# Performance work log

Hardware: AMD Instinct MI355X
Metric: run time of the kernel (lower is better)

Reference implementation:

```python
import jax, jax.numpy as jnp
import numpy as np
from jax import lax

N, H, W = 8, 64, 64
SX1, SX2, THX, TLX = 256, 256, 256, 256
E1, E2, A1, OT = 256, 64, 128, 256
EBD = SX2 // 2            # ebd_factor=2
TXC = THX + TLX           # 512
IN1 = SX1 + TXC           # 768
BV = EBD + TXC            # 640


def upsample2x_align_corners(x):
    # bilinear, align_corners=True, scale_factor=2 (matches nn.Upsample)
    n, c, h, w = x.shape
    ho, wo = 2 * h, 2 * w
    ys = jnp.linspace(0.0, h - 1.0, ho)
    xs = jnp.linspace(0.0, w - 1.0, wo)
    y0 = jnp.floor(ys).astype(jnp.int32); y1 = jnp.minimum(y0 + 1, h - 1)
    x0 = jnp.floor(xs).astype(jnp.int32); x1 = jnp.minimum(x0 + 1, w - 1)
    wy = (ys - y0).astype(x.dtype); wx = (xs - x0).astype(x.dtype)
    xh = x[:, :, y0, :] * (1.0 - wy)[None, None, :, None] + x[:, :, y1, :] * wy[None, None, :, None]
    return xh[:, :, :, x0] * (1.0 - wx) + xh[:, :, :, x1] * wx


def conv1x1(x, w, b=None):
    # x: [N,C,H,W], w: [O,C]
    y = jnp.einsum('nchw,oc->nohw', x, w)
    if b is not None:
        y = y + b[None, :, None, None]
    return y


def conv3x3(x, w, b):
    y = lax.conv_general_dilated(x, w, window_strides=(1, 1), padding=((1, 1), (1, 1)),
                                 dimension_numbers=('NCHW', 'OIHW', 'NCHW'))
    return y + b[None, :, None, None]


def setup_inputs() -> dict:
    key = jax.random.key(0)
    ks = jax.random.split(key, 20)
    g = lambda k, shape, fan: jax.random.normal(k, shape, jnp.float32) * np.sqrt(2.0 / fan)
    return {
        'sx1': jax.random.normal(ks[0], (N, SX1, H, W), jnp.float32),
        'sx2': jax.random.normal(ks[1], (N, SX2, H, W), jnp.float32),
        't_hx': jax.random.normal(ks[2], (N, THX, H, W), jnp.float32),
        'tx': jax.random.normal(ks[3], (N, TLX, H // 2, W // 2), jnp.float32),
        'W_t1': g(ks[4], (E1, IN1), IN1 + E1), 'b_t1': jnp.zeros((E1,), jnp.float32),
        'W_t2': g(ks[5], (E2, E1), E1 + E2),
        'W_t3': g(ks[6], (SX2, E2), E2 + SX2),
        'W_U': g(ks[7], (SX2, SX2), 2 * SX2), 'b_U': jnp.zeros((SX2,), jnp.float32),
        'W_V': g(ks[8], (EBD, SX2), SX2 + EBD), 'b_V': jnp.zeros((EBD,), jnp.float32),
        'W_a1': g(ks[9], (A1, BV), BV + A1), 'b_a1': jnp.zeros((A1,), jnp.float32),
        'W_a2': g(ks[10], (BV, A1), A1 + BV), 'b_a2': jnp.zeros((BV,), jnp.float32),
        'W_ot': g(ks[11], (OT, BV, 3, 3), 9 * (BV + OT)), 'b_ot': jnp.zeros((OT,), jnp.float32),
    }


def reference(sx1, sx2, t_hx, tx, W_t1, b_t1, W_t2, W_t3, W_U, b_U, W_V, b_V,
              W_a1, b_a1, W_a2, b_a2, W_ot, b_ot):
    tx_up = upsample2x_align_corners(tx)
    txc = jnp.concatenate([t_hx, tx_up], axis=1)          # [N,TXC,H,W]
    st = jnp.concatenate([sx1, txc], axis=1)              # [N,IN1,H,W]
    w = jax.nn.relu(conv1x1(st, W_t1, b_t1))
    w = jnp.mean(w, axis=(2, 3), keepdims=True)           # GAP -> [N,E1,1,1]
    w = jax.nn.relu(conv1x1(w, W_t2))
    w = conv1x1(w, W_t3)                                  # [N,SX2,1,1]
    norm = jnp.sqrt(jnp.sum(w * w, axis=1, keepdims=True))
    w = w / jnp.maximum(norm, 1e-12)                      # F.normalize(dim=1)
    b = jax.nn.relu(conv1x1(sx2, W_U, b_U))
    b = b * w                                             # AdaptiveConv2d grouped 1x1 == per-sample per-channel scale
    b = jax.nn.relu(conv1x1(b, W_V, b_V))
    b = jnp.concatenate([b, txc], axis=1)                 # [N,BV,H,W]
    a = jax.nn.relu(conv1x1(b, W_a1, b_a1))
    a = jax.nn.sigmoid(conv1x1(a, W_a2, b_a2))
    a = a * b
    a = jax.nn.relu(conv3x3(a, W_ot, b_ot))               # [N,OT,H,W]
    return (a, w)
```

## Files before the change

kernel.cpp:

```cpp
#include <hip/hip_runtime.h>
#include <hip/hip_bf16.h>

#define PP 4096
#define HH 64
#define WW 64

typedef __attribute__((ext_vector_type(8))) short short8b;
typedef __attribute__((ext_vector_type(4))) float f32x4;

static __device__ __forceinline__ float bf2f(short s) {
    union { unsigned int u; float f; } cv; cv.u = ((unsigned int)(unsigned short)s) << 16; return cv.f;
}
static __device__ __forceinline__ short f2bf(float f) {
    __hip_bfloat16 h = __float2bfloat16(f);
    return *reinterpret_cast<short*>(&h);
}

static __device__ __forceinline__ void pack16(const float* __restrict__ W,
                                              short* __restrict__ dst,
                                              int MT, int K, int s) {
    int total = MT * 2 * (K / 64) * 64;
    if (s >= total) return;
    int lane = s & 63;
    int rest = s >> 6;
    int ks = rest & 1; rest >>= 1;
    int mt = rest % MT;
    int cc = rest / MT;
    int o   = mt * 16 + (lane & 15);
    int ch0 = cc * 64 + ks * 32 + (lane >> 4) * 8;
    short8b v;
    #pragma unroll
    for (int j = 0; j < 8; ++j) v[j] = f2bf(W[(size_t)o * K + ch0 + j]);
    ((short8b*)dst)[s] = v;
}

__global__ void k_packall(const float* __restrict__ Wt1, const float* __restrict__ WU,
                          const float* __restrict__ WV, const float* __restrict__ Wa1,
                          const float* __restrict__ Wa2, const float* __restrict__ Wot,
                          short* __restrict__ Wt1p, short* __restrict__ WUp,
                          short* __restrict__ WVp, short* __restrict__ Wa1p,
                          short* __restrict__ Wa2p, short* __restrict__ Wotp) {
    int b = blockIdx.x, tid = threadIdx.x;
    if (b < 96)       { pack16(Wt1, Wt1p, 16, 768, (b)       * 256 + tid); }
    else if (b < 128) { pack16(WU,  WUp,  16, 256, (b - 96)  * 256 + tid); }
    else if (b < 144) { pack16(WV,  WVp,   8, 256, (b - 128) * 256 + tid); }
    else if (b < 184) { pack16(Wa1, Wa1p,  8, 640, (b - 144) * 256 + tid); }
    else if (b < 224) { pack16(Wa2, Wa2p, 40, 128, (b - 184) * 256 + tid); }
    else {
        int s = (b - 224) * 256 + tid;
        int lane = s & 63;
        int rest = s >> 6;
        int ks = rest & 1;  rest >>= 1;
        int mt = rest & 15; rest >>= 4;
        int cc = rest % 10;
        int k9 = rest / 10;
        int o   = mt * 16 + (lane & 15);
        int ch0 = cc * 64 + ks * 32 + (lane >> 4) * 8;
        short8b v{};
        #pragma unroll
        for (int j = 0; j < 8; ++j)
            v[j] = f2bf(Wot[((size_t)o * 640 + ch0 + j) * 9 + k9]);
        ((short8b*)Wotp)[s] = v;
    }
}

__global__ void k_t2h_all(const float* __restrict__ t_hx, const float* __restrict__ tx,
                          short* __restrict__ txc, short* __restrict__ txh) {
    __shared__ short T[64 * 65];
    int tid = threadIdx.x;
    int by = blockIdx.y;
    const float* src; short* dst; int P, pitch, yb;
    if (by < 4)  { src = t_hx; dst = txc; P = 4096; pitch = 512; yb = by; }
    else { if (blockIdx.x >= 16) return;
           src = tx;   dst = txh; P = 1024; pitch = 256; yb = by - 4; }
    int p0 = blockIdx.x * 64, c0 = yb * 64, n = blockIdx.z;
    #pragma unroll
    for (int it = 0; it < 16; ++it) {
        int slot = it * 256 + tid;
        int ch = slot >> 6, px = slot & 63;
        T[ch * 65 + px] = f2bf(src[((size_t)(n * 256 + c0 + ch)) * P + p0 + px]);
    }
    __syncthreads();
    #pragma unroll
    for (int it = 0; it < 16; ++it) {
        int slot = it * 256 + tid;
        int px = slot >> 6, ch = slot & 63;
        dst[((size_t)n * P + p0 + px) * pitch + c0 + ch] = T[ch * 65 + px];
    }
}

__global__ void k_up(const short* __restrict__ txh, short* __restrict__ txc) {
    int tid = threadIdx.x;
    int cg = tid & 31, pxl = tid >> 5;
    int px = blockIdx.x * 8 + pxl;
    int n  = blockIdx.z;
    int y = px >> 6, x = px & 63;
    const float s = 31.0f / 63.0f;
    float fy = y * s, fx = x * s;
    int y0 = (int)fy, x0 = (int)fx;
    int y1 = min(y0 + 1, 31), x1 = min(x0 + 1, 31);
    float wy = fy - (float)y0, wx = fx - (float)x0;
    const short8b* base = (const short8b*)(txh + ((size_t)n * 1024) * 256);
    short8b a = base[((size_t)(y0 * 32 + x0) * 256 + cg * 8) >> 3];
    short8b b = base[((size_t)(y0 * 32 + x1) * 256 + cg * 8) >> 3];
    short8b c = base[((size_t)(y1 * 32 + x0) * 256 + cg * 8) >> 3];
    short8b d = base[((size_t)(y1 * 32 + x1) * 256 + cg * 8) >> 3];
    short8b r;
    #pragma unroll
    for (int j = 0; j < 8; ++j) {
        float v = (bf2f(a[j]) * (1.f - wy) + bf2f(c[j]) * wy) * (1.f - wx)
                + (bf2f(b[j]) * (1.f - wy) + bf2f(d[j]) * wy) * wx;
        r[j] = f2bf(v);
    }
    *(short8b*)(txc + ((size_t)n * PP + px) * 512 + 256 + cg * 8) = r;
}

static __device__ __forceinline__ void stage64(const short* __restrict__ src, int pitch,
                                               int c0, size_t rowbase, short* lds, int tid) {
    #pragma unroll
    for (int it = 0; it < 4; ++it) {
        int idx = it * 256 + tid;
        int px = idx >> 3, cg = idx & 7;
        short8b v = *(const short8b*)(src + (rowbase + px) * (size_t)pitch + c0 + cg * 8);
        int elem = (px * 64 + cg * 8) ^ ((px & 7) << 3);
        *(short8b*)&lds[elem] = v;
    }
}
static __device__ __forceinline__ void stage64f(const float* __restrict__ ten, int C,
                                                int c0, int n, int pxbase,
                                                short* lds, int tid) {
    int chp = tid & 31;
    int pxg = tid >> 5;
    const float* p0 = ten + ((size_t)(n * C + c0 + chp * 2)) * PP + pxbase + pxg * 16;
    const float* p1 = p0 + PP;
    #pragma unroll
    for (int kq = 0; kq < 4; ++kq) {
        f32x4 a = *(const f32x4*)(p0 + kq * 4);
        f32x4 b = *(const f32x4*)(p1 + kq * 4);
        #pragma unroll
        for (int j = 0; j < 4; ++j) {
            int px = pxg * 16 + kq * 4 + j;
            int idx = px * 64 + ((chp * 2) ^ ((px & 7) << 3));
            unsigned int u = (unsigned int)(unsigned short)f2bf(a[j])
                           | ((unsigned int)(unsigned short)f2bf(b[j]) << 16);
            *(unsigned int*)&lds[idx] = u;
        }
    }
}
static __device__ __forceinline__ short8b afrag(const short* lds, int pw, int mf, int ks, int lane) {
    int px = pw * 64 + mf * 16 + (lane & 15);
    int elem = (px * 64 + ks * 32 + ((lane >> 4) * 8)) ^ ((px & 7) << 3);
    return *(const short8b*)&lds[elem];
}
#define GEMM_PROLOG \
    int tid = threadIdx.x, lane = tid & 63, wid = tid >> 6; \
    int pw = wid & 1, ow = wid >> 1; \
    int bx = blockIdx.y, pt = blockIdx.x, n = blockIdx.z; \
    size_t rowbase = (size_t)n * PP + pt * 128; \
    f32x4 acc[4][4] = {}; (void)bx; (void)rowbase;
#define GEMM_STEP(MT) { \
    short8b afr[4][2], bfr[4][2]; \
    _Pragma("unroll") for (int mf = 0; mf < 4; ++mf) \
        _Pragma("unroll") for (int ks = 0; ks < 2; ++ks) afr[mf][ks] = afrag(lds, pw, mf, ks, lane); \
    _Pragma("unroll") for (int nf = 0; nf < 4; ++nf) { \
        int mt_g = bx * 8 + ow * 4 + nf; \
        _Pragma("unroll") for (int ks = 0; ks < 2; ++ks) \
            bfr[nf][ks] = wfv[(((size_t)cc * (MT) + mt_g) * 2 + ks) * 64 + lane]; } \
    _Pragma("unroll") for (int ks = 0; ks < 2; ++ks) \
        _Pragma("unroll") for (int mf = 0; mf < 4; ++mf) \
            _Pragma("unroll") for (int nf = 0; nf < 4; ++nf) \
                acc[mf][nf] = __builtin_amdgcn_mfma_f32_16x16x32_bf16(afr[mf][ks], bfr[nf][ks], acc[mf][nf], 0, 0, 0); }

__global__ __launch_bounds__(256) void k_gemm_gap(const float* __restrict__ sx1,
        const short* __restrict__ txc, const short* __restrict__ wf,
        const float* __restrict__ bias, float* __restrict__ part) {
    __shared__ short lds[128 * 64];
    __shared__ float red[128 * 2];
    GEMM_PROLOG
    const short8b* wfv = (const short8b*)wf;
    for (int cc = 0; cc < 12; ++cc) {
        __syncthreads();
        if (cc < 4) stage64f(sx1, 256, cc * 64, n, pt * 128, lds, tid);
        else        stage64(txc, 512, (cc - 4) * 64, rowbase, lds, tid);
        __syncthreads();
        GEMM_STEP(16)
    }
    #pragma unroll
    for (int nf = 0; nf < 4; ++nf) {
        int o = bx * 128 + ow * 64 + nf * 16 + (lane & 15);
        float b = bias[o];
        float s = 0.f;
        #pragma unroll
        for (int mf = 0; mf < 4; ++mf)
            #pragma unroll
            for (int r = 0; r < 4; ++r) {
                float v = acc[mf][nf][r] + b;
                s += v > 0.f ? v : 0.f;
            }
        s += __shfl_xor(s, 16);
        s += __shfl_xor(s, 32);
        if (lane < 16) red[(ow * 64 + nf * 16 + lane) * 2 + pw] = s;
    }
    __syncthreads();
    if (tid < 128)
        part[((size_t)n * 256 + bx * 128 + tid) * 32 + pt] = red[tid * 2] + red[tid * 2 + 1];
}

__global__ __launch_bounds__(256) void k_gemm_bU(const float* __restrict__ sx2,
        const short* __restrict__ wf, const float* __restrict__ bias,
        const float* __restrict__ wvec, short* __restrict__ bUh) {
    __shared__ short lds[128 * 64];
    GEMM_PROLOG
    const short8b* wfv = (const short8b*)wf;
    for (int cc = 0; cc < 4; ++cc) {
        __syncthreads();
        stage64f(sx2, 256, cc * 64, n, pt * 128, lds, tid);
        __syncthreads();
        GEMM_STEP(16)
    }
    #pragma unroll
    for (int nf = 0; nf < 4; ++nf) {
        int o = bx * 128 + ow * 64 + nf * 16 + (lane & 15);
        float b = bias[o], wv = wvec[n * 256 + o];
        #pragma unroll
        for (int mf = 0; mf < 4; ++mf)
            #pragma unroll
            for (int r = 0; r < 4; ++r) {
                int px = pw * 64 + mf * 16 + (lane >> 4) * 4 + r;
                float v = acc[mf][nf][r] + b;
                v = v > 0.f ? v : 0.f;
                bUh[(rowbase + px) * 256 + o] = f2bf(v * wv);
            }
    }
}

__global__ __launch_bounds__(256) void k_gemm_bV(const short* __restrict__ bUh,
        const short* __restrict__ wf, const float* __restrict__ bias,
        short* __restrict__ bVh) {
    __shared__ short lds[128 * 64];
    GEMM_PROLOG
    const short8b* wfv = (const short8b*)wf;
    for (int cc = 0; cc < 4; ++cc) {
        __syncthreads();
        stage64(bUh, 256, cc * 64, rowbase, lds, tid);
        __syncthreads();
        GEMM_STEP(8)
    }
    #pragma unroll
    for (int nf = 0; nf < 4; ++nf) {
        int o = ow * 64 + nf * 16 + (lane & 15);
        float b = bias[o];
        #pragma unroll
        for (int mf = 0; mf < 4; ++mf)
            #pragma unroll
            for (int r = 0; r < 4; ++r) {
                int px = pw * 64 + mf * 16 + (lane >> 4) * 4 + r;
                float v = acc[mf][nf][r] + b;
                bVh[(rowbase + px) * 128 + o] = f2bf(v > 0.f ? v : 0.f);
            }
    }
}

__global__ __launch_bounds__(256) void k_gemm_a1(const short* __restrict__ bVh,
        const short* __restrict__ txc, const short* __restrict__ wf,
        const float* __restrict__ bias, short* __restrict__ a1h) {
    __shared__ short lds[128 * 64];
    GEMM_PROLOG
    const short8b* wfv = (const short8b*)wf;
    for (int cc = 0; cc < 10; ++cc) {
        __syncthreads();
        if (cc < 2) stage64(bVh, 128, cc * 64, rowbase, lds, tid);
        else        stage64(txc, 512, (cc - 2) * 64, rowbase, lds, tid);
        __syncthreads();
        GEMM_STEP(8)
    }
    #pragma unroll
    for (int nf = 0; nf < 4; ++nf) {
        int o = ow * 64 + nf * 16 + (lane & 15);
        float b = bias[o];
        #pragma unroll
        for (int mf = 0; mf < 4; ++mf)
            #pragma unroll
            for (int r = 0; r < 4; ++r) {
                int px = pw * 64 + mf * 16 + (lane >> 4) * 4 + r;
                float v = acc[mf][nf][r] + b;
                a1h[(rowbase + px) * 128 + o] = f2bf(v > 0.f ? v : 0.f);
            }
    }
}

__global__ __launch_bounds__(256) void k_gemm_amul(const short* __restrict__ a1h,
        const short* __restrict__ wf, const float* __restrict__ bias,
        const short* __restrict__ bVh, const short* __restrict__ txc,
        short* __restrict__ amulH) {
    __shared__ short lds[128 * 64];
    GEMM_PROLOG
    const short8b* wfv = (const short8b*)wf;
    for (int cc = 0; cc < 2; ++cc) {
        __syncthreads();
        stage64(a1h, 128, cc * 64, rowbase, lds, tid);
        __syncthreads();
        GEMM_STEP(40)
    }
    #pragma unroll
    for (int nf = 0; nf < 4; ++nf) {
        int o = bx * 128 + ow * 64 + nf * 16 + (lane & 15);
        float b = bias[o];
        #pragma unroll
        for (int mf = 0; mf < 4; ++mf)
            #pragma unroll
            for (int r = 0; r < 4; ++r) {
                int px = pw * 64 + mf * 16 + (lane >> 4) * 4 + r;
                float xv = acc[mf][nf][r] + b;
                float sg = 1.0f / (1.0f + expf(-xv));
                float bval = (o < 128) ? bf2f(bVh[(rowbase + px) * 128 + o])
                                       : bf2f(txc[(rowbase + px) * 512 + o - 128]);
                amulH[(rowbase + px) * 640 + o] = f2bf(sg * bval);
            }
    }
}

__global__ void k_wvec(const float* __restrict__ part, const float* __restrict__ Wt2,
                       const float* __restrict__ Wt3, float* __restrict__ wvec,
                       float* __restrict__ out_w) {
    int n = blockIdx.x, tid = threadIdx.x;
    __shared__ float sm1[256];
    __shared__ float sm2[64];
    __shared__ float smr[4];
    float s = 0.0f;
    #pragma unroll
    for (int t = 0; t < 32; ++t) s += part[(size_t)(n * 256 + tid) * 32 + t];
    sm1[tid] = s * (1.0f / 4096.0f);
    __syncthreads();
    if (tid < 64) {
        float a = 0.0f;
        for (int c = 0; c < 256; ++c) a = fmaf(Wt2[tid * 256 + c], sm1[c], a);
        sm2[tid] = a > 0.0f ? a : 0.0f;
    }
    __syncthreads();
    float w3 = 0.0f;
    for (int e = 0; e < 64; ++e) w3 = fmaf(Wt3[tid * 64 + e], sm2[e], w3);
    float q = w3 * w3;
    int lane = tid & 63, wv = tid >> 6;
    #pragma unroll
    for (int off = 32; off > 0; off >>= 1) q += __shfl_down(q, off);
    if (lane == 0) smr[wv] = q;
    __syncthreads();
    float nrm = sqrtf(smr[0] + smr[1] + smr[2] + smr[3]);
    nrm = fmaxf(nrm, 1e-12f);
    float w = w3 / nrm;
    wvec[n * 256 + tid] = w;
    out_w[n * 256 + tid] = w;
}

#define WLOAD(dst, u, kss) { \
    _Pragma("unroll") for (int mf = 0; mf < 4; ++mf) { \
        int mt_g = bx * 8 + mw * 4 + mf; \
        dst[mf] = wf[(((size_t)(u) * 16 + mt_g) * 2 + (kss)) * 64 + lane]; } }

#define BLOAD(dst, kyv, kxv, ksv) { \
    _Pragma("unroll") for (int nf = 0; nf < 4; ++nf) { \
        int col = nf * 16 + (lane & 15); \
        int chc = col + (kxv); \
        int row_eff = nw + (kyv); \
        int elem = ((row_eff * 66 + chc) * 64 + (ksv) * 32 + (lane >> 4) * 8) \
                   ^ ((chc & 7) << 3); \
        dst[nf] = *(const short8b*)&lds_x[elem]; } }

#define MFMA16(W, B) { \
    _Pragma("unroll") for (int mf = 0; mf < 4; ++mf) \
        _Pragma("unroll") for (int nf = 0; nf < 4; ++nf) \
            acc[mf][nf] = __builtin_amdgcn_mfma_f32_16x16x32_bf16( \
                W[mf], B[nf], acc[mf][nf], 0, 0, 0); }

__global__ __launch_bounds__(512, 1) void k_conv3_mfma(
        const short* __restrict__ amulH, const short* __restrict__ Wfrag,
        const float* __restrict__ bot, float* __restrict__ out_a) {
    __shared__ short lds_x[6 * 66 * 64];
    const int tid  = threadIdx.x;
    const int lane = tid & 63;
    const int wid  = tid >> 6;
    const int mw = wid & 1;
    const int nw = wid >> 1;
    const int qx = blockIdx.x;
    const int bx = blockIdx.y;
    const int n  = blockIdx.z;

    f32x4 acc[4][4] = {};
    const short8b* wf = (const short8b*)Wfrag;

    const int scol = tid >> 3, scg = tid & 7;
    short8b vreg[6];
    #pragma unroll
    for (int it = 0; it < 6; ++it) {
        int gr = qx * 4 - 1 + it;
        short8b t{};
        if (gr >= 0 && gr < 64)
            t = *(const short8b*)(amulH + ((size_t)(n * PP + gr * 64 + scol)) * 640 + scg * 8);
        vreg[it] = t;
    }
    if (tid < 96) {
        int rr = tid >> 4, side = (tid >> 3) & 1, cg = tid & 7;
        int chc = side ? 65 : 0;
        int elem = ((rr * 66 + chc) * 64 + cg * 8) ^ ((chc & 7) << 3);
        *(short8b*)&lds_x[elem] = short8b{};
    }

    short8b wA[4], wB[4], bfrA[4], bfrB[4];
    WLOAD(wA, 0, 0)

    for (int cc = 0; cc < 10; ++cc) {
        __syncthreads();
        {
            int chc = scol + 1;
            #pragma unroll
            for (int it = 0; it < 6; ++it) {
                int elem = ((it * 66 + chc) * 64 + scg * 8) ^ ((chc & 7) << 3);
                *(short8b*)&lds_x[elem] = vreg[it];
            }
        }
        __syncthreads();
        if (cc < 9) {
            #pragma unroll
            for (int it = 0; it < 6; ++it) {
                int gr = qx * 4 - 1 + it;
                short8b t{};
                if (gr >= 0 && gr < 64)
                    t = *(const short8b*)(amulH + ((size_t)(n * PP + gr * 64 + scol)) * 640
                                          + (cc + 1) * 64 + scg * 8);
                vreg[it] = t;
            }
        }
        BLOAD(bfrA, 0, 0, 0)
        #pragma unroll
        for (int h = 0; h < 18; ++h) {
            const bool even = ((h & 1) == 0);
            if (h < 17) {
                const int hn = h + 1;
                const int k9n = hn >> 1, ksn = hn & 1;
                const int kyn = k9n / 3, kxn = k9n % 3;
                const int un = k9n * 10 + cc;
                if (even) { BLOAD(bfrB, kyn, kxn, ksn) WLOAD(wB, un, ksn) }
                else      { BLOAD(bfrA, kyn, kxn, ksn) WLOAD(wA, un, ksn) }
            } else {
                WLOAD(wA, cc + 1, 0)
            }
            if (even) { MFMA16(wA, bfrA) } else { MFMA16(wB, bfrB) }
        }
    }
    #pragma unroll
    for (int mf = 0; mf < 4; ++mf) {
        int o = bx * 128 + mw * 64 + mf * 16 + (lane >> 4) * 4;
        #pragma unroll
        for (int r = 0; r < 4; ++r) {
            float bias = bot[o + r];
            #pragma unroll
            for (int nf = 0; nf < 4; ++nf) {
                int p = qx * 256 + nw * 64 + nf * 16 + (lane & 15);
                float v = acc[mf][nf][r] + bias;
                out_a[((size_t)(n * 256 + o + r)) * PP + p] = v > 0.f ? v : 0.f;
            }
        }
    }
}

extern "C" void kernel_launch(void* const* d_in, const int* in_sizes, int n_in,
                              void* d_out, int out_size, void* d_ws, size_t ws_size,
                              hipStream_t stream) {
    static const int want[18] = {
        8388608, 8388608, 8388608, 2097152, 196608, 256, 16384, 16384,
        65536, 256, 32768, 128, 81920, 128, 81920, 640, 1474560, 256
    };
    const void* ptr[18];
    bool used[64];
    for (int i = 0; i < 64; ++i) used[i] = false;
    bool ok = (n_in >= 18 && n_in <= 64);
    for (int k = 0; k < 18 && ok; ++k) {
        ptr[k] = nullptr;
        for (int i = 0; i < n_in; ++i) {
            if (!used[i] && in_sizes[i] == want[k]) { ptr[k] = d_in[i]; used[i] = true; break; }
        }
        if (!ptr[k]) ok = false;
    }
    if (!ok) { for (int k = 0; k < 18; ++k) ptr[k] = d_in[k]; }

    const float* sx1  = (const float*)ptr[0];
    const float* sx2  = (const float*)ptr[1];
    const float* t_hx = (const float*)ptr[2];
    const float* tx   = (const float*)ptr[3];
    const float* Wt1  = (const float*)ptr[4];
    const float* bt1  = (const float*)ptr[5];
    const float* Wt2  = (const float*)ptr[6];
    const float* Wt3  = (const float*)ptr[7];
    const float* WU   = (const float*)ptr[8];
    const float* bU   = (const float*)ptr[9];
    const float* WV   = (const float*)ptr[10];
    const float* bV   = (const float*)ptr[11];
    const float* Wa1  = (const float*)ptr[12];
    const float* ba1  = (const float*)ptr[13];
    const float* Wa2  = (const float*)ptr[14];
    const float* ba2  = (const float*)ptr[15];
    const float* Wot  = (const float*)ptr[16];
    const float* bot  = (const float*)ptr[17];

    char* base = (char*)d_ws;
    short* txc   = (short*)base;
    short* bUh   = (short*)(base + (size_t)33554432);
    short* amulH = (short*)(base + (size_t)33554432);
    short* txh   = (short*)(base + (size_t)75497472);
    short* bVh   = (short*)(base + (size_t)75497472);
    short* a1h   = (short*)(base + (size_t)83886080);
    float* part  = (float*)(base + (size_t)92274688);
    float* wvec  = (float*)(base + (size_t)92536832);
    short* Wt1p  = (short*)(base + (size_t)92545024);
    short* WUp   = (short*)(base + (size_t)92938240);
    short* WVp   = (short*)(base + (size_t)93069312);
    short* Wa1p  = (short*)(base + (size_t)93134848);
    short* Wa2p  = (short*)(base + (size_t)93298688);
    short* Wotp  = (short*)(base + (size_t)93462528);

    float* out_a = (float*)d_out;
    float* out_w = out_a + (size_t)8 * 256 * PP;

    k_packall<<<dim3(944), 256, 0, stream>>>(Wt1, WU, WV, Wa1, Wa2, Wot,
                                             Wt1p, WUp, WVp, Wa1p, Wa2p, Wotp);
    k_t2h_all<<<dim3(64, 8, 8), 256, 0, stream>>>(t_hx, tx, txc, txh);
    k_up<<<dim3(512, 1, 8), 256, 0, stream>>>(txh, txc);

    k_gemm_gap <<<dim3(32, 2, 8), 256, 0, stream>>>(sx1, txc, Wt1p, bt1, part);
    k_wvec     <<<dim3(8),        256, 0, stream>>>(part, Wt2, Wt3, wvec, out_w);
    k_gemm_bU  <<<dim3(32, 2, 8), 256, 0, stream>>>(sx2, WUp, bU, wvec, bUh);
    k_gemm_bV  <<<dim3(32, 1, 8), 256, 0, stream>>>(bUh, WVp, bV, bVh);
    k_gemm_a1  <<<dim3(32, 1, 8), 256, 0, stream>>>(bVh, txc, Wa1p, ba1, a1h);
    k_gemm_amul<<<dim3(32, 5, 8), 256, 0, stream>>>(a1h, Wa2p, ba2, bVh, txc, amulH);
    k_conv3_mfma<<<dim3(16, 2, 8), 512, 0, stream>>>(amulH, Wotp, bot, out_a);
}
```

Before: 267.9 us.

## Fuse a1 GEMM and sigmoid-gated a2 GEMM into one kernel via LDS

Combines the a1 conv GEMM and the a2 GEMM with its sigmoid-multiply epilogue into a single kernel. The relu'd a1 tile is kept in swizzled LDS instead of being written to and reread from global memory, and the a2 GEMM loops over all five output column blocks inside each workgroup. This removes one launch and the a1h round trip. In exchange the grid shrinks from 1280 to 256 workgroups, each doing five times the a2 work serially, and LDS use rises to 48KB per block, which may hurt occupancy and latency hiding.

```diff
diff --git a/kernel.cpp b/kernel.cpp
--- a/kernel.cpp
+++ b/kernel.cpp
@@ -261,62 +261,82 @@
     }
 }
 
-__global__ __launch_bounds__(256) void k_gemm_a1(const short* __restrict__ bVh,
-        const short* __restrict__ txc, const short* __restrict__ wf,
-        const float* __restrict__ bias, short* __restrict__ a1h) {
+__global__ __launch_bounds__(256) void k_gemm_a1amul(const short* __restrict__ bVh,
+        const short* __restrict__ txc, const short* __restrict__ wf1,
+        const float* __restrict__ b1, const short* __restrict__ wf2,
+        const float* __restrict__ b2, short* __restrict__ amulH) {
     __shared__ short lds[128 * 64];
+    __shared__ short a1l[2][128 * 64];
     GEMM_PROLOG
-    const short8b* wfv = (const short8b*)wf;
-    for (int cc = 0; cc < 10; ++cc) {
-        __syncthreads();
-        if (cc < 2) stage64(bVh, 128, cc * 64, rowbase, lds, tid);
-        else        stage64(txc, 512, (cc - 2) * 64, rowbase, lds, tid);
-        __syncthreads();
-        GEMM_STEP(8)
+    {
+        const short8b* wfv = (const short8b*)wf1;
+        for (int cc = 0; cc < 10; ++cc) {
+            __syncthreads();
+            if (cc < 2) stage64(bVh, 128, cc * 64, rowbase, lds, tid);
+            else        stage64(txc, 512, (cc - 2) * 64, rowbase, lds, tid);
+            __syncthreads();
+            GEMM_STEP(8)
+        }
     }
     #pragma unroll
     for (int nf = 0; nf < 4; ++nf) {
-        int o = ow * 64 + nf * 16 + (lane & 15);
-        float b = bias[o];
+        int oo = ow * 64 + nf * 16 + (lane & 15);
+        float b = b1[oo];
         #pragma unroll
         for (int mf = 0; mf < 4; ++mf)
             #pragma unroll
             for (int r = 0; r < 4; ++r) {
                 int px = pw * 64 + mf * 16 + (lane >> 4) * 4 + r;
                 float v = acc[mf][nf][r] + b;
-                a1h[(rowbase + px) * 128 + o] = f2bf(v > 0.f ? v : 0.f);
-            }
-    }
-}
-
-__global__ __launch_bounds__(256) void k_gemm_amul(const short* __restrict__ a1h,
-        const short* __restrict__ wf, const float* __restrict__ bias,
-        const short* __restrict__ bVh, const short* __restrict__ txc,
-        short* __restrict__ amulH) {
-    __shared__ short lds[128 * 64];
-    GEMM_PROLOG
-    const short8b* wfv = (const short8b*)wf;
-    for (int cc = 0; cc < 2; ++cc) {
-        __syncthreads();
-        stage64(a1h, 128, cc * 64, rowbase, lds, tid);
-        __syncthreads();
-        GEMM_STEP(40)
-    }
-    #pragma unroll
-    for (int nf = 0; nf < 4; ++nf) {
-        int o = bx * 128 + ow * 64 + nf * 16 + (lane & 15);
-        float b = bias[o];
-        #pragma unroll
-        for (int mf = 0; mf < 4; ++mf)
-            #pragma unroll
-            for (int r = 0; r < 4; ++r) {
-                int px = pw * 64 + mf * 16 + (lane >> 4) * 4 + r;
-                float xv = acc[mf][nf][r] + b;
-                float sg = 1.0f / (1.0f + expf(-xv));
-                float bval = (o < 128) ? bf2f(bVh[(rowbase + px) * 128 + o])
-                                       : bf2f(txc[(rowbase + px) * 512 + o - 128]);
-                amulH[(rowbase + px) * 640 + o] = f2bf(sg * bval);
-            }
+                v = v > 0.f ? v : 0.f;
+                int ch = oo & 63;
+                a1l[oo >> 6][px * 64 + (ch ^ ((px & 7) << 3))] = f2bf(v);
+            }
+    }
+    __syncthreads();
+    const short8b* wfv2 = (const short8b*)wf2;
+    for (int bx5 = 0; bx5 < 5; ++bx5) {
+        f32x4 acc2[4][4] = {};
+        #pragma unroll
+        for (int cc = 0; cc < 2; ++cc) {
+            short8b afr[4][2], bfr[4][2];
+            #pragma unroll
+            for (int mf = 0; mf < 4; ++mf)
+                #pragma unroll
+                for (int ks = 0; ks < 2; ++ks)
+                    afr[mf][ks] = afrag(a1l[cc], pw, mf, ks, lane);
+            #pragma unroll
+            for (int nf = 0; nf < 4; ++nf) {
+                int mt_g = bx5 * 8 + ow * 4 + nf;
+                #pragma unroll
+                for (int ks = 0; ks < 2; ++ks)
+                    bfr[nf][ks] = wfv2[(((size_t)cc * 40 + mt_g) * 2 + ks) * 64 + lane];
+            }
+            #pragma unroll
+            for (int ks = 0; ks < 2; ++ks)
+                #pragma unroll
+                for (int mf = 0; mf < 4; ++mf)
+                    #pragma unroll
+                    for (int nf = 0; nf < 4; ++nf)
+                        acc2[mf][nf] = __builtin_amdgcn_mfma_f32_16x16x32_bf16(
+                            afr[mf][ks], bfr[nf][ks], acc2[mf][nf], 0, 0, 0);
+        }
+        #pragma unroll
+        for (int nf = 0; nf < 4; ++nf) {
+            int o = bx5 * 128 + ow * 64 + nf * 16 + (lane & 15);
+            float b = b2[o];
+            #pragma unroll
+            for (int mf = 0; mf < 4; ++mf)
+                #pragma unroll
+                for (int r = 0; r < 4; ++r) {
+                    int px = pw * 64 + mf * 16 + (lane >> 4) * 4 + r;
+                    float xv = acc2[mf][nf][r] + b;
+                    float sg = 1.0f / (1.0f + expf(-xv));
+                    float bval = (o < 128) ? bf2f(bVh[(rowbase + px) * 128 + o])
+                                           : bf2f(txc[(rowbase + px) * 512 + o - 128]);
+                    amulH[(rowbase + px) * 640 + o] = f2bf(sg * bval);
+                }
+        }
     }
 }
 
@@ -509,7 +529,6 @@
     short* amulH = (short*)(base + (size_t)33554432);
     short* txh   = (short*)(base + (size_t)75497472);
     short* bVh   = (short*)(base + (size_t)75497472);
-    short* a1h   = (short*)(base + (size_t)83886080);
     float* part  = (float*)(base + (size_t)92274688);
     float* wvec  = (float*)(base + (size_t)92536832);
     short* Wt1p  = (short*)(base + (size_t)92545024);
@@ -531,7 +550,7 @@
     k_wvec     <<<dim3(8),        256, 0, stream>>>(part, Wt2, Wt3, wvec, out_w);
     k_gemm_bU  <<<dim3(32, 2, 8), 256, 0, stream>>>(sx2, WUp, bU, wvec, bUh);
     k_gemm_bV  <<<dim3(32, 1, 8), 256, 0, stream>>>(bUh, WVp, bV, bVh);
-    k_gemm_a1  <<<dim3(32, 1, 8), 256, 0, stream>>>(bVh, txc, Wa1p, ba1, a1h);
-    k_gemm_amul<<<dim3(32, 5, 8), 256, 0, stream>>>(a1h, Wa2p, ba2, bVh, txc, amulH);
+    k_gemm_a1amul<<<dim3(32, 1, 8), 256, 0, stream>>>(bVh, txc, Wa1p, ba1,
+                                                      Wa2p, ba2, amulH);
     k_conv3_mfma<<<dim3(16, 2, 8), 512, 0, stream>>>(amulH, Wotp, bot, out_a);
 }
```

After: 303.4 us. +13.3%, slower.
